# Optimization experiments

Measured on AMD Instinct MI355X. Metric: run time of the kernel, lower is better.

The kernel has to match this reference:

```python
import jax, jax.numpy as jnp
import numpy as np

D, NH, HD, NL, NP, DFF = 256, 8, 32, 4, 4, 1024
B, LQ = 16, 900
SHAPES = np.array([[100, 100], [50, 50], [25, 25], [13, 13]], dtype=np.int64)
_AREAS = SHAPES[:, 0] * SHAPES[:, 1]
LSI = np.concatenate([[0], np.cumsum(_AREAS)[:-1]]).astype(np.int64)
S = int(_AREAS.sum())  # 13294


def setup_inputs() -> dict:
    key = jax.random.key(0)
    ki = iter(jax.random.split(key, 40))
    def nrm(shape, s=1.0):
        return jax.random.normal(next(ki), shape, jnp.float32) * s
    p = dict(
        tgt=nrm((B, LQ, D)),
        query_pos=nrm((B, LQ, D)) * 0.1,
        reference_points=jax.random.uniform(next(ki), (B, LQ, NL, 2), jnp.float32),
        src=nrm((B, S, D)),
        src_spatial_shapes=SHAPES,
        level_start_index=LSI,
        src_padding_mask=np.zeros((B, S), dtype=bool),
        Wq=nrm((D, D), 0.02), bq=jnp.zeros((D,)),
        Wk=nrm((D, D), 0.02), bk=jnp.zeros((D,)),
        Wv=nrm((D, D), 0.02), bv=jnp.zeros((D,)),
        Wo=nrm((D, D), 0.02), bo=jnp.zeros((D,)),
        g2=jnp.ones((D,)), be2=jnp.zeros((D,)),
        Woff=nrm((D, NH * NL * NP * 2), 0.02),
        boff=jax.random.uniform(next(ki), (NH * NL * NP * 2,), jnp.float32, -0.5, 0.5),
        Waw=nrm((D, NH * NL * NP), 0.02), baw=jnp.zeros((NH * NL * NP,)),
        Wval=nrm((D, D), 0.02), bval=jnp.zeros((D,)),
        Wout=nrm((D, D), 0.02), bout=jnp.zeros((D,)),
        g1=jnp.ones((D,)), be1=jnp.zeros((D,)),
        W1f=nrm((D, DFF), 0.02), b1f=jnp.zeros((DFF,)),
        W2f=nrm((DFF, D), 0.02), b2f=jnp.zeros((D,)),
        g3=jnp.ones((D,)), be3=jnp.zeros((D,)),
    )
    return p


def layernorm(x, g, b):
    m = jnp.mean(x, -1, keepdims=True)
    v = jnp.var(x, -1, keepdims=True)
    return (x - m) * jax.lax.rsqrt(v + 1e-5) * g + b


def reference(tgt, query_pos, reference_points, src, src_spatial_shapes,
              level_start_index, src_padding_mask,
              Wq, bq, Wk, bk, Wv, bv, Wo, bo, g2, be2,
              Woff, boff, Waw, baw, Wval, bval, Wout, bout, g1, be1,
              W1f, b1f, W2f, b2f, g3, be3):
    Bq, Lq, _ = tgt.shape
    # ---- self-attention (q = k = tgt + pos, v = tgt), dropout in eval = identity
    q = tgt + query_pos
    qh = (q @ Wq + bq).reshape(Bq, Lq, NH, HD)
    kh = (q @ Wk + bk).reshape(Bq, Lq, NH, HD)
    vh = (tgt @ Wv + bv).reshape(Bq, Lq, NH, HD)
    att = jax.nn.softmax(jnp.einsum('bqhd,bkhd->bhqk', qh, kh) / np.sqrt(HD), axis=-1)
    sa = jnp.einsum('bhqk,bkhd->bqhd', att, vh).reshape(Bq, Lq, D) @ Wo + bo
    tgt = layernorm(tgt + sa, g2, be2)
    # ---- multi-scale deformable cross-attention
    query = tgt + query_pos
    value = src @ Wval + bval
    value = jnp.where(jnp.asarray(src_padding_mask)[..., None], 0.0, value)
    value = value.reshape(Bq, -1, NH, HD)
    off = (query @ Woff + boff).reshape(Bq, Lq, NH, NL, NP, 2)
    aw = jax.nn.softmax((query @ Waw + baw).reshape(Bq, Lq, NH, NL * NP), axis=-1)
    aw = aw.reshape(Bq, Lq, NH, NL, NP)
    ss = np.asarray(src_spatial_shapes)
    lsi = np.asarray(level_start_index)
    norm = jnp.asarray(ss[:, ::-1].astype(np.float32))  # (W, H) per level
    # sampling locations in [0,1]: [B, Lq, NH, NL, NP, 2]
    loc = reference_points[:, :, None, :, None, :] + off / norm[None, None, None, :, None, :]
    out = jnp.zeros((Bq, NH, Lq, HD), value.dtype)
    for l in range(NL):
        Hc, Wc = int(ss[l, 0]), int(ss[l, 1])
        v2 = value[:, lsi[l]:lsi[l] + Hc * Wc].transpose(0, 2, 1, 3)  # [B, NH, H*W, HD]
        x = loc[:, :, :, l, :, 0] * Wc - 0.5  # [B, Lq, NH, NP] (align_corners=False)
        y = loc[:, :, :, l, :, 1] * Hc - 0.5
        x0 = jnp.floor(x); y0 = jnp.floor(y)
        lx = x - x0; ly = y - y0
        x0i = x0.astype(jnp.int32); y0i = y0.astype(jnp.int32)
        samp = jnp.zeros((Bq, NH, Lq * NP, HD), value.dtype)
        for dy, dx, w in ((0, 0, (1 - ly) * (1 - lx)), (0, 1, (1 - ly) * lx),
                          (1, 0, ly * (1 - lx)), (1, 1, ly * lx)):
            xi = x0i + dx; yi = y0i + dy
            valid = (xi >= 0) & (xi < Wc) & (yi >= 0) & (yi < Hc)  # zero padding
            idx = jnp.clip(yi, 0, Hc - 1) * Wc + jnp.clip(xi, 0, Wc - 1)
            idx2 = idx.transpose(0, 2, 1, 3).reshape(Bq, NH, Lq * NP)
            g = jnp.take_along_axis(v2, idx2[..., None], axis=2)  # [B, NH, Lq*NP, HD]
            wv = (w * valid).transpose(0, 2, 1, 3).reshape(Bq, NH, Lq * NP)
            samp = samp + wv[..., None] * g
        samp = samp.reshape(Bq, NH, Lq, NP, HD)
        out = out + jnp.einsum('bqhp,bhqpd->bhqd', aw[:, :, :, l, :], samp)
    ca = out.transpose(0, 2, 1, 3).reshape(Bq, Lq, D) @ Wout + bout
    tgt = layernorm(tgt + ca, g1, be1)
    # ---- FFN
    ff = jax.nn.relu(tgt @ W1f + b1f) @ W2f + b2f
    return layernorm(tgt + ff, g3, be3)
```

## Files before the change

kernel.cpp:

```cpp
#include <hip/hip_runtime.h>
#include <math.h>

#define DD 256
#define NH 8
#define HD 32
#define NL 4
#define NP 4
#define DFF 1024
#define BB 16
#define LQ 900
#define S_TOT 13294

#define M1   (BB * LQ)
#define MP1  14464
#define MV   (BB * S_TOT)
#define MPV  212736

typedef unsigned short u16;
typedef unsigned int   u32;
typedef __attribute__((ext_vector_type(8))) short s8v;
typedef __attribute__((ext_vector_type(4))) float f32x4;

__constant__ int c_H[NL]    = {100, 50, 25, 13};
__constant__ int c_W[NL]    = {100, 50, 25, 13};
__constant__ int c_base[NL] = {0, 10000, 12500, 13125};

__device__ __forceinline__ float b2f(u16 u) {
    return __uint_as_float(((u32)u) << 16);
}
__device__ __forceinline__ u16 f2b(float f) {
    u32 x = __float_as_uint(f);
    u32 r = x + 0x7fffu + ((x >> 16) & 1u);
    return (u16)(r >> 16);
}
__device__ __forceinline__ u32 pk2(float a, float b) {
    return (u32)f2b(a) | ((u32)f2b(b) << 16);
}
__device__ __forceinline__ void gload16(const u16* g, u16* ldsbase) {
    __builtin_amdgcn_global_load_lds(
        (const __attribute__((address_space(1))) unsigned int*)(const void*)g,
        (__attribute__((address_space(3))) unsigned int*)(void*)ldsbase,
        16, 0, 0);
}
__device__ __forceinline__ int2 xcd_swizzle()
{
    int nwg  = gridDim.x * gridDim.y;
    int orig = blockIdx.y * gridDim.x + blockIdx.x;
    int q = nwg >> 3, r = nwg & 7;
    int xcd = orig & 7, pos = orig >> 3;
    int wg = (xcd < r ? xcd * (q + 1) : r * (q + 1) + (xcd - r) * q) + pos;
    int2 res;
    res.x = wg % gridDim.x;
    res.y = wg / gridDim.x;
    return res;
}

#define OFF_QK   0
#define OFF_V    131072
#define OFF_O    196608
#define OFF_VAL  262144
#define OFF_OUT  327680
#define OFF_OA   393216
#define OFF_F1   491520
#define OFF_F2   753664
#define WTS_TOT  1015808

__global__ __launch_bounds__(256)
void prep_kernel(const float* __restrict__ Wq, const float* __restrict__ Wk,
                 const float* __restrict__ Wv, const float* __restrict__ Wo,
                 const float* __restrict__ Wval, const float* __restrict__ Wout,
                 const float* __restrict__ Woff, const float* __restrict__ Waw,
                 const float* __restrict__ W1f, const float* __restrict__ W2f,
                 const float* __restrict__ pbq, const float* __restrict__ pbk,
                 const float* __restrict__ boff, const float* __restrict__ baw,
                 u16* __restrict__ WTS, float* __restrict__ bqk, float* __restrict__ boa)
{
    int t = blockIdx.x;
    if (t >= 992) {
        if (t == 992) {
            for (int i = threadIdx.x; i < 512; i += 256)
                bqk[i] = (i < 256) ? pbq[i] : pbk[i - 256];
        } else {
            for (int i = threadIdx.x; i < 384; i += 256)
                boa[i] = (i < 256) ? boff[i] : baw[i - 256];
        }
        return;
    }
    const float* src; u16* dst; int K, N, tt;
    if (t < 448) {
        int wsel = t >> 6; tt = t & 63;
        const float* srcs[7] = {Wq, Wk, Wv, Wo, Wval, Wout, Woff};
        const int   offs[7]  = {OFF_QK, OFF_QK + 65536, OFF_V, OFF_O, OFF_VAL, OFF_OUT, OFF_OA};
        src = srcs[wsel]; dst = WTS + offs[wsel]; K = 256; N = 256;
    } else if (t < 480) {
        tt = t - 448; src = Waw; dst = WTS + OFF_OA + 65536; K = 256; N = 128;
    } else if (t < 736) {
        tt = t - 480; src = W1f; dst = WTS + OFF_F1; K = 256; N = 1024;
    } else {
        tt = t - 736; src = W2f; dst = WTS + OFF_F2; K = 1024; N = 256;
    }
    int nt = N / 32;
    int n0 = (tt % nt) * 32, k0 = (tt / nt) * 32;

    __shared__ float tb[32][33];
    int tx = threadIdx.x & 31, ty = threadIdx.x >> 5;
    #pragma unroll
    for (int i = 0; i < 4; ++i) {
        int k = ty + i * 8;
        tb[k][tx] = src[(size_t)(k0 + k) * N + n0 + tx];
    }
    __syncthreads();
    #pragma unroll
    for (int i = 0; i < 4; ++i) {
        int n = ty + i * 8;
        dst[(size_t)(n0 + n) * K + k0 + tx] = f2b(tb[tx][n]);
    }
}

__global__ __launch_bounds__(256)
void acvt2_kernel(const float* __restrict__ tgt, const float* __restrict__ qpos,
                  u16* __restrict__ B0, u16* __restrict__ B1)
{
    int i8 = blockIdx.x * 256 + threadIdx.x;
    int row = i8 >> 5;
    uint4 o0, o1;
    if (row < M1) {
        const float4* tp = (const float4*)(tgt + (size_t)i8 * 8);
        const float4* pp = (const float4*)(qpos + (size_t)i8 * 8);
        float4 t0 = tp[0], t1 = tp[1], p0 = pp[0], p1 = pp[1];
        o1.x = pk2(t0.x, t0.y); o1.y = pk2(t0.z, t0.w);
        o1.z = pk2(t1.x, t1.y); o1.w = pk2(t1.z, t1.w);
        o0.x = pk2(t0.x + p0.x, t0.y + p0.y); o0.y = pk2(t0.z + p0.z, t0.w + p0.w);
        o0.z = pk2(t1.x + p1.x, t1.y + p1.y); o0.w = pk2(t1.z + p1.z, t1.w + p1.w);
    } else {
        o0.x = o0.y = o0.z = o0.w = 0;
        o1 = o0;
    }
    ((uint4*)B0)[i8] = o0;
    ((uint4*)B1)[i8] = o1;
}

template<int BNT, int OUTBF, int RELU>
__global__ __launch_bounds__(256)
void mgemm(const u16* __restrict__ A, const u16* __restrict__ Bt,
           const float* __restrict__ bias, void* __restrict__ Cv,
           int K, int N, int Mreal)
{
    constexpr int MF = (BNT == 128) ? 4 : 2;
    __shared__ u16 Asu[2][128 * 32];
    __shared__ u16 Bsu[2][BNT * 32];

    int2 sw = xcd_swizzle();
    int tid = threadIdx.x;
    int w = tid >> 6, l = tid & 63;
    int mbase = (BNT == 128) ? (w >> 1) * 64 : w * 32;
    int nbase = (BNT == 128) ? (w & 1) * 64 : 0;
    long m0 = (long)sw.y * 128;
    int n0 = sw.x * BNT;

    f32x4 acc[MF][4];
    #pragma unroll
    for (int i = 0; i < MF; ++i)
        #pragma unroll
        for (int j = 0; j < 4; ++j) {
            acc[i][j][0] = 0.f; acc[i][j][1] = 0.f;
            acc[i][j][2] = 0.f; acc[i][j][3] = 0.f;
        }

    int lr = l & 15, lk = (l >> 4) * 8;
    int srow = l >> 2;
    int scol = (l & 3) * 8;

    auto stage = [&](int buf, int k0) {
        if (BNT == 128) {
            #pragma unroll
            for (int j = 0; j < 2; ++j) {
                int row = w * 32 + j * 16;
                gload16(Bt + (size_t)(n0 + row + srow) * K + k0 + scol, &Bsu[buf][row * 32]);
            }
        } else {
            int row = w * 16;
            gload16(Bt + (size_t)(n0 + row + srow) * K + k0 + scol, &Bsu[buf][row * 32]);
        }
        #pragma unroll
        for (int j = 0; j < 2; ++j) {
            int row = w * 32 + j * 16;
            gload16(A + (m0 + row + srow) * (long)K + k0 + scol, &Asu[buf][row * 32]);
        }
    };

    int nsteps = K >> 5;
    stage(0, 0);
    __syncthreads();

    int cur = 0;
    for (int s = 0; s < nsteps; ++s) {
        if (s + 1 < nsteps) stage(cur ^ 1, (s + 1) * 32);
        s8v af[MF], bf[4];
        #pragma unroll
        for (int mi = 0; mi < MF; ++mi)
            af[mi] = *(const s8v*)(Asu[cur] + (mbase + mi * 16 + lr) * 32 + lk);
        #pragma unroll
        for (int nj = 0; nj < 4; ++nj)
            bf[nj] = *(const s8v*)(Bsu[cur] + (nbase + nj * 16 + lr) * 32 + lk);
        #pragma unroll
        for (int mi = 0; mi < MF; ++mi)
            #pragma unroll
            for (int nj = 0; nj < 4; ++nj)
                acc[mi][nj] = __builtin_amdgcn_mfma_f32_16x16x32_bf16(
                    af[mi], bf[nj], acc[mi][nj], 0, 0, 0);
        __syncthreads();
        cur ^= 1;
    }

    int lq = l >> 4;
    #pragma unroll
    for (int nj = 0; nj < 4; ++nj) {
        int col = n0 + nbase + nj * 16 + lr;
        float bv = bias[col];
        #pragma unroll
        for (int mi = 0; mi < MF; ++mi) {
            #pragma unroll
            for (int r = 0; r < 4; ++r) {
                long row = m0 + mbase + mi * 16 + lq * 4 + r;
                float v = acc[mi][nj][r] + bv;
                if (RELU) v = fmaxf(v, 0.f);
                if (OUTBF) ((u16*)Cv)[row * N + col] = f2b(v);
                else       ((float*)Cv)[row * N + col] = v;
            }
        }
    }
}

__global__ __launch_bounds__(256)
void vgemm(const float* __restrict__ A, const u16* __restrict__ Bt,
           const float* __restrict__ bias, u16* __restrict__ C, int Mreal)
{
    const int K = 256, N = 256;
    __shared__ u16 Asu[64 * 32];
    __shared__ u16 Bsu[128 * 32];

    int2 sw = xcd_swizzle();
    int tid = threadIdx.x;
    int w = tid >> 6, l = tid & 63;
    int wr = w >> 1, wc = w & 1;
    long m0 = (long)sw.y * 64;
    int n0 = sw.x * 128;

    f32x4 acc[2][4];
    #pragma unroll
    for (int i = 0; i < 2; ++i)
        #pragma unroll
        for (int j = 0; j < 4; ++j) {
            acc[i][j][0] = 0.f; acc[i][j][1] = 0.f;
            acc[i][j][2] = 0.f; acc[i][j][3] = 0.f;
        }

    int lr = l & 15, lk = (l >> 4) * 8;
    int srow = l >> 2, scol = (l & 3) * 8;

    for (int k0 = 0; k0 < K; k0 += 32) {
        #pragma unroll
        for (int j = 0; j < 2; ++j) {
            int row = w * 32 + j * 16;
            gload16(Bt + (size_t)(n0 + row + srow) * K + k0 + scol, &Bsu[row * 32]);
        }
        int c = tid;
        #pragma unroll
        for (int it = 0; it < 2; ++it) {
            int row = c >> 3, col = (c & 7) * 4;
            long gr = m0 + row;
            if (gr >= Mreal) gr = Mreal - 1;
            float4 v = *(const float4*)(A + gr * K + k0 + col);
            ushort4 o;
            o.x = f2b(v.x); o.y = f2b(v.y); o.z = f2b(v.z); o.w = f2b(v.w);
            ((ushort4*)Asu)[c] = o;
            c += 256;
        }
        __syncthreads();
        s8v af[2], bf[4];
        #pragma unroll
        for (int mi = 0; mi < 2; ++mi)
            af[mi] = *(const s8v*)(Asu + (wr * 32 + mi * 16 + lr) * 32 + lk);
        #pragma unroll
        for (int nj = 0; nj < 4; ++nj)
            bf[nj] = *(const s8v*)(Bsu + (wc * 64 + nj * 16 + lr) * 32 + lk);
        #pragma unroll
        for (int mi = 0; mi < 2; ++mi)
            #pragma unroll
            for (int nj = 0; nj < 4; ++nj)
                acc[mi][nj] = __builtin_amdgcn_mfma_f32_16x16x32_bf16(
                    af[mi], bf[nj], acc[mi][nj], 0, 0, 0);
        __syncthreads();
    }

    int lq = l >> 4;
    #pragma unroll
    for (int nj = 0; nj < 4; ++nj) {
        int col = n0 + wc * 64 + nj * 16 + lr;
        float bv = bias[col];
        #pragma unroll
        for (int mi = 0; mi < 2; ++mi) {
            #pragma unroll
            for (int r = 0; r < 4; ++r) {
                long row = m0 + wr * 32 + mi * 16 + lq * 4 + r;
                C[row * N + col] = f2b(acc[mi][nj][r] + bv);
            }
        }
    }
}

#define QT 64
#define KT2 64
#define KSP 48
#define VSP 40
#define PSP 72
__global__ __launch_bounds__(256)
void mattn(const u16* __restrict__ qk, const u16* __restrict__ vh,
           u16* __restrict__ sa)
{
    __shared__ u16 Ks[KT2][KSP];
    __shared__ u32 Vt32[32][VSP];
    __shared__ u16 Ps[4][16][PSP];

    int tid = threadIdx.x;
    int w = tid >> 6, l = tid & 63;
    int lr = l & 15, hi = l >> 4;
    int b = blockIdx.x >> 3, h = blockIdx.x & 7;
    int q0 = blockIdx.y * QT + w * 16;

    s8v qf;
    {
        s8v raw = *(const s8v*)(qk + ((size_t)(b * LQ + q0 + lr) * 512) + h * HD + hi * 8);
        #pragma unroll
        for (int j = 0; j < 8; ++j)
            raw[j] = (short)f2b(b2f((u16)raw[j]) * 0.17677669529663687f);
        qf = raw;
    }

    f32x4 o0 = {0.f,0.f,0.f,0.f}, o1 = {0.f,0.f,0.f,0.f};
    float lrun[4] = {0.f,0.f,0.f,0.f};

    const u16* kbase = qk + (size_t)b * LQ * 512 + 256 + h * HD;
    const u16* vbase = vh + (size_t)b * LQ * 256 + h * HD;

    int krow = tid >> 2, kc8 = (tid & 3) * 8;
    int k2 = tid & 31, d0 = (tid >> 5) * 4;

    for (int kb = 0; kb < LQ; kb += KT2) {
        int gk = kb + krow;        if (gk >= LQ) gk = LQ - 1;
        int gv0 = kb + 2 * k2;     if (gv0 >= LQ) gv0 = LQ - 1;
        int gv1 = kb + 2 * k2 + 1; if (gv1 >= LQ) gv1 = LQ - 1;
        uint4 kv = *(const uint4*)(kbase + (size_t)gk * 512 + kc8);
        uint2 va = *(const uint2*)(vbase + (size_t)gv0 * 256 + d0);
        uint2 vb = *(const uint2*)(vbase + (size_t)gv1 * 256 + d0);
        __syncthreads();
        *(uint4*)(&Ks[krow][kc8]) = kv;
        Vt32[d0 + 0][k2] = (va.x & 0xffffu)      | (vb.x << 16);
        Vt32[d0 + 1][k2] = (va.x >> 16)          | (vb.x & 0xffff0000u);
        Vt32[d0 + 2][k2] = (va.y & 0xffffu)      | (vb.y << 16);
        Vt32[d0 + 3][k2] = (va.y >> 16)          | (vb.y & 0xffff0000u);
        __syncthreads();

        f32x4 s[4];
        #pragma unroll
        for (int kk = 0; kk < 4; ++kk) {
            s8v bk = *(const s8v*)(&Ks[kk * 16 + lr][hi * 8]);
            f32x4 z = {0.f,0.f,0.f,0.f};
            s[kk] = __builtin_amdgcn_mfma_f32_16x16x32_bf16(qf, bk, z, 0, 0, 0);
        }
        if (kb + KT2 > LQ) {
            #pragma unroll
            for (int kk = 0; kk < 4; ++kk)
                if (kb + kk * 16 + lr >= LQ) {
                    s[kk][0] = -1e30f; s[kk][1] = -1e30f;
                    s[kk][2] = -1e30f; s[kk][3] = -1e30f;
                }
        }

        #pragma unroll
        for (int r = 0; r < 4; ++r) {
            float p0 = __expf(s[0][r]);
            float p1 = __expf(s[1][r]);
            float p2 = __expf(s[2][r]);
            float p3 = __expf(s[3][r]);
            lrun[r] += (p0 + p1) + (p2 + p3);
            int qr = hi * 4 + r;
            Ps[w][qr][lr]      = f2b(p0);
            Ps[w][qr][16 + lr] = f2b(p1);
            Ps[w][qr][32 + lr] = f2b(p2);
            Ps[w][qr][48 + lr] = f2b(p3);
        }

        s8v ap0  = *(const s8v*)(&Ps[w][lr][hi * 8]);
        s8v ap1  = *(const s8v*)(&Ps[w][lr][32 + hi * 8]);
        s8v bv00 = *(const s8v*)(&Vt32[lr][hi * 4]);
        s8v bv10 = *(const s8v*)(&Vt32[lr][16 + hi * 4]);
        s8v bv01 = *(const s8v*)(&Vt32[16 + lr][hi * 4]);
        s8v bv11 = *(const s8v*)(&Vt32[16 + lr][16 + hi * 4]);
        o0 = __builtin_amdgcn_mfma_f32_16x16x32_bf16(ap0, bv00, o0, 0, 0, 0);
        o0 = __builtin_amdgcn_mfma_f32_16x16x32_bf16(ap1, bv10, o0, 0, 0, 0);
        o1 = __builtin_amdgcn_mfma_f32_16x16x32_bf16(ap0, bv01, o1, 0, 0, 0);
        o1 = __builtin_amdgcn_mfma_f32_16x16x32_bf16(ap1, bv11, o1, 0, 0, 0);
    }

    #pragma unroll
    for (int r = 0; r < 4; ++r) {
        float ps = lrun[r];
        ps += __shfl_xor(ps, 1);
        ps += __shfl_xor(ps, 2);
        ps += __shfl_xor(ps, 4);
        ps += __shfl_xor(ps, 8);
        int q = q0 + hi * 4 + r;
        if (q < LQ) {
            float inv = 1.f / ps;
            u16* op = sa + (size_t)(b * LQ + q) * DD + h * HD;
            op[lr]      = f2b(o0[r] * inv);
            op[16 + lr] = f2b(o1[r] * inv);
        }
    }
}

__global__ __launch_bounds__(256)
void ln_kernel(const float* __restrict__ x, const u16* __restrict__ y,
               const float* __restrict__ g, const float* __restrict__ be,
               float* __restrict__ out, const float* __restrict__ pos,
               u16* __restrict__ bfout, int M)
{
    int wave = threadIdx.x >> 6;
    int lane = threadIdx.x & 63;
    int row = blockIdx.x * 4 + wave;
    if (row >= M) return;
    float4 xv = ((const float4*)(x + (size_t)row * DD))[lane];
    ushort4 yv = ((const ushort4*)(y + (size_t)row * DD))[lane];
    float v[4] = {xv.x + b2f(yv.x), xv.y + b2f(yv.y),
                  xv.z + b2f(yv.z), xv.w + b2f(yv.w)};
    float s = v[0] + v[1] + v[2] + v[3];
    float sq = v[0]*v[0] + v[1]*v[1] + v[2]*v[2] + v[3]*v[3];
    for (int o = 32; o; o >>= 1) {
        s += __shfl_xor(s, o);
        sq += __shfl_xor(sq, o);
    }
    float mean = s * (1.f / DD);
    float var = sq * (1.f / DD) - mean * mean;
    float r = rsqrtf(var + 1e-5f);
    float4 gv = ((const float4*)g)[lane];
    float4 bv = ((const float4*)be)[lane];
    float4 ov;
    ov.x = (v[0] - mean) * r * gv.x + bv.x;
    ov.y = (v[1] - mean) * r * gv.y + bv.y;
    ov.z = (v[2] - mean) * r * gv.z + bv.z;
    ov.w = (v[3] - mean) * r * gv.w + bv.w;
    ((float4*)(out + (size_t)row * DD))[lane] = ov;
    if (bfout) {
        float4 pv = make_float4(0.f, 0.f, 0.f, 0.f);
        if (pos) pv = ((const float4*)(pos + (size_t)row * DD))[lane];
        ushort4 bo;
        bo.x = f2b(ov.x + pv.x); bo.y = f2b(ov.y + pv.y);
        bo.z = f2b(ov.z + pv.z); bo.w = f2b(ov.w + pv.w);
        ((ushort4*)(bfout + (size_t)row * DD))[lane] = bo;
    }
}

__global__ __launch_bounds__(256)
void sample_kernel(const float* __restrict__ offaw, const float* __restrict__ refp,
                   const u16* __restrict__ value, u16* __restrict__ out)
{
    __shared__ float2 sPW[2][128][4];
    int t = threadIdx.x;
    int sub = t >> 7;
    int bq = blockIdx.x * 2 + sub;
    int b = bq / LQ;

    {
        int pt = t & 127;
        int h = pt >> 4, j = pt & 15, l = j >> 2, p = j & 3;
        const float* row = offaw + (size_t)bq * 384;
        float lg = row[256 + h * 16 + j];
        float mx = lg;
        mx = fmaxf(mx, __shfl_xor(mx, 1));
        mx = fmaxf(mx, __shfl_xor(mx, 2));
        mx = fmaxf(mx, __shfl_xor(mx, 4));
        mx = fmaxf(mx, __shfl_xor(mx, 8));
        float e = __expf(lg - mx);
        float se = e;
        se += __shfl_xor(se, 1);
        se += __shfl_xor(se, 2);
        se += __shfl_xor(se, 4);
        se += __shfl_xor(se, 8);
        float aw = e / se;

        float ox = row[h * 32 + l * 8 + p * 2 + 0];
        float oy = row[h * 32 + l * 8 + p * 2 + 1];
        int Hc = c_H[l], Wc = c_W[l];
        float x = refp[(size_t)bq * 8 + l * 2 + 0] * Wc + ox - 0.5f;
        float y = refp[(size_t)bq * 8 + l * 2 + 1] * Hc + oy - 0.5f;
        float x0f = floorf(x), y0f = floorf(y);
        float lx = x - x0f, ly = y - y0f;
        int x0 = (int)x0f, y0 = (int)y0f;
        int vb = (b * S_TOT + c_base[l]) * 128;
        #pragma unroll
        for (int c = 0; c < 4; ++c) {
            int dy = c >> 1, dx = c & 1;
            int xi = x0 + dx, yi = y0 + dy;
            bool ok = (xi >= 0) & (xi < Wc) & (yi >= 0) & (yi < Hc);
            float wgt = (dy ? ly : 1.f - ly) * (dx ? lx : 1.f - lx) * aw;
            float2 pw;
            pw.x = __int_as_float(ok ? vb + (yi * Wc + xi) * 128 : 0);
            pw.y = ok ? wgt : 0.f;
            sPW[sub][pt][c] = pw;
        }
    }
    __syncthreads();

    {
        int s = t & 127;
        int h = s >> 4, d2 = s & 15;
        const u32* v32 = (const u32*)value;
        int lane = h * 16 + d2;
        float a0 = 0.f, a1 = 0.f;
        #pragma unroll
        for (int j = 0; j < 16; ++j) {
            #pragma unroll
            for (int c = 0; c < 4; ++c) {
                float2 pw = sPW[sub][h * 16 + j][c];
                u32 pv = v32[__float_as_int(pw.x) + lane];
                a0 += pw.y * __uint_as_float(pv << 16);
                a1 += pw.y * __uint_as_float(pv & 0xffff0000u);
            }
        }
        *(u32*)(out + (size_t)bq * DD + h * 32 + d2 * 2) = pk2(a0, a1);
    }
}

extern "C" void kernel_launch(void* const* d_in, const int* in_sizes, int n_in,
                              void* d_out, int out_size, void* d_ws, size_t ws_size,
                              hipStream_t stream)
{
    const float* tgt  = (const float*)d_in[0];
    const float* qpos = (const float*)d_in[1];
    const float* refp = (const float*)d_in[2];
    const float* src  = (const float*)d_in[3];
    const float* Wq  = (const float*)d_in[7];
    const float* pbq = (const float*)d_in[8];
    const float* Wk  = (const float*)d_in[9];
    const float* pbk = (const float*)d_in[10];
    const float* Wv  = (const float*)d_in[11];
    const float* pbv = (const float*)d_in[12];
    const float* Wo  = (const float*)d_in[13];
    const float* pbo = (const float*)d_in[14];
    const float* g2  = (const float*)d_in[15];
    const float* be2 = (const float*)d_in[16];
    const float* Woff = (const float*)d_in[17];
    const float* boff = (const float*)d_in[18];
    const float* Waw  = (const float*)d_in[19];
    const float* baw  = (const float*)d_in[20];
    const float* Wval = (const float*)d_in[21];
    const float* bval = (const float*)d_in[22];
    const float* Wout = (const float*)d_in[23];
    const float* bout = (const float*)d_in[24];
    const float* g1   = (const float*)d_in[25];
    const float* be1  = (const float*)d_in[26];
    const float* W1f  = (const float*)d_in[27];
    const float* b1f  = (const float*)d_in[28];
    const float* W2f  = (const float*)d_in[29];
    const float* b2f_ = (const float*)d_in[30];
    const float* g3   = (const float*)d_in[31];
    const float* be3  = (const float*)d_in[32];

    char* base = (char*)d_ws;
    size_t off = 0;
    auto alloc = [&](size_t bytes) -> void* {
        void* p = base + off;
        off = (off + bytes + 255) & ~(size_t)255;
        return p;
    };
    const size_t AB = (size_t)MP1 * DD * sizeof(u16);
    u16* B0  = (u16*)alloc(AB);
    u16* B1  = (u16*)alloc(AB);
    u16* BQK = (u16*)alloc((size_t)MP1 * 512 * sizeof(u16));
    u16* B4  = (u16*)alloc(AB);
    u16* TMPB= (u16*)alloc(AB);
    u16* FFH = (u16*)alloc((size_t)MP1 * DFF * sizeof(u16));
    u16* VAL = (u16*)alloc((size_t)MPV * DD * sizeof(u16));
    float* F0 = (float*)alloc((size_t)MP1 * 384 * sizeof(float));
    float* F2 = (float*)alloc((size_t)MP1 * DD * sizeof(float));
    float* F3 = (float*)alloc((size_t)MP1 * DD * sizeof(float));
    u16* WTS = (u16*)alloc((size_t)WTS_TOT * sizeof(u16));
    float* bqk = (float*)alloc(512 * sizeof(float));
    float* boa = (float*)alloc(384 * sizeof(float));

    dim3 blk(256);

    prep_kernel<<<dim3(994), blk, 0, stream>>>(
        Wq, Wk, Wv, Wo, Wval, Wout, Woff, Waw, W1f, W2f,
        pbq, pbk, boff, baw, WTS, bqk, boa);

    const int MT = MP1 / 128;
    const dim3 gval(2, MPV / 64);
    const dim3 g512b(8,  MT);
    const dim3 g256b(4,  MT);
    const dim3 g384b(6,  MT);
    const dim3 g1kb(16,  MT);

    acvt2_kernel<<<dim3(MP1 * 32 / 256), blk, 0, stream>>>(tgt, qpos, B0, B1);
    mgemm<64,1,0><<<g512b, blk, 0, stream>>>(B0, WTS + OFF_QK, bqk, BQK, DD, 512, M1);
    mgemm<64,1,0><<<g256b, blk, 0, stream>>>(B1, WTS + OFF_V, pbv, B4, DD, DD, M1);
    mattn<<<dim3(BB * NH, (LQ + QT - 1) / QT), blk, 0, stream>>>(BQK, B4, B0);
    mgemm<64,1,0><<<g256b, blk, 0, stream>>>(B0, WTS + OFF_O, pbo, TMPB, DD, DD, M1);
    ln_kernel<<<dim3(M1 / 4), blk, 0, stream>>>(tgt, TMPB, g2, be2, F2, qpos, B1, M1);

    vgemm<<<gval, blk, 0, stream>>>(src, WTS + OFF_VAL, bval, VAL, MV);
    mgemm<64,0,0><<<g384b, blk, 0, stream>>>(B1, WTS + OFF_OA, boa, F0, DD, 384, M1);
    sample_kernel<<<dim3(M1 / 2), blk, 0, stream>>>(F0, refp, VAL, B4);
    mgemm<64,1,0><<<g256b, blk, 0, stream>>>(B4, WTS + OFF_OUT, bout, TMPB, DD, DD, M1);
    ln_kernel<<<dim3(M1 / 4), blk, 0, stream>>>(F2, TMPB, g1, be1, F3, nullptr, B1, M1);

    mgemm<64,1,1><<<g1kb, blk, 0, stream>>>(B1, WTS + OFF_F1, b1f, FFH, DD, DFF, M1);
    mgemm<64,1,0><<<g256b, blk, 0, stream>>>(FFH, WTS + OFF_F2, b2f_, TMPB, DFF, DD, M1);
    ln_kernel<<<dim3(M1 / 4), blk, 0, stream>>>(F3, TMPB, g3, be3, (float*)d_out, nullptr, nullptr, M1);
}
```

Before: 313.8 us.

## Widen deformable sampling gathers to 8 bytes and split points across half-warps

The sampling kernel now gathers four bf16 channels per 8-byte load instead of two per 4-byte load. Each thread handles half of a head's 16 sampling points, and the two halves are combined through a shared-memory reduction with an extra block barrier. This is meant to cut the number of scattered gather instructions while keeping thread-level parallelism. The self-attention kernel also raises wave priority around its MFMA blocks with s_setprio, so matrix work is issued ahead of other waves' memory traffic.

After: 320.0 us. Within noise of the previous version (+2.0%).

```diff
diff --git a/kernel.cpp b/kernel.cpp
--- a/kernel.cpp
+++ b/kernel.cpp
@@ -363,12 +363,14 @@
         __syncthreads();
 
         f32x4 s[4];
+        __builtin_amdgcn_s_setprio(1);
         #pragma unroll
         for (int kk = 0; kk < 4; ++kk) {
             s8v bk = *(const s8v*)(&Ks[kk * 16 + lr][hi * 8]);
             f32x4 z = {0.f,0.f,0.f,0.f};
             s[kk] = __builtin_amdgcn_mfma_f32_16x16x32_bf16(qf, bk, z, 0, 0, 0);
         }
+        __builtin_amdgcn_s_setprio(0);
         if (kb + KT2 > LQ) {
             #pragma unroll
             for (int kk = 0; kk < 4; ++kk)
@@ -398,10 +400,12 @@
         s8v bv10 = *(const s8v*)(&Vt32[lr][16 + hi * 4]);
         s8v bv01 = *(const s8v*)(&Vt32[16 + lr][hi * 4]);
         s8v bv11 = *(const s8v*)(&Vt32[16 + lr][16 + hi * 4]);
+        __builtin_amdgcn_s_setprio(1);
         o0 = __builtin_amdgcn_mfma_f32_16x16x32_bf16(ap0, bv00, o0, 0, 0, 0);
         o0 = __builtin_amdgcn_mfma_f32_16x16x32_bf16(ap1, bv10, o0, 0, 0, 0);
         o1 = __builtin_amdgcn_mfma_f32_16x16x32_bf16(ap0, bv01, o1, 0, 0, 0);
         o1 = __builtin_amdgcn_mfma_f32_16x16x32_bf16(ap1, bv11, o1, 0, 0, 0);
+        __builtin_amdgcn_s_setprio(0);
     }
 
     #pragma unroll
@@ -467,6 +471,7 @@
                    const u16* __restrict__ value, u16* __restrict__ out)
 {
     __shared__ float2 sPW[2][128][4];
+    __shared__ float4 sRed[2][64];
     int t = threadIdx.x;
     int sub = t >> 7;
     int bq = blockIdx.x * 2 + sub;
@@ -498,7 +503,7 @@
         float x0f = floorf(x), y0f = floorf(y);
         float lx = x - x0f, ly = y - y0f;
         int x0 = (int)x0f, y0 = (int)y0f;
-        int vb = (b * S_TOT + c_base[l]) * 128;
+        int vb = (b * S_TOT + c_base[l]) * 64;
         #pragma unroll
         for (int c = 0; c < 4; ++c) {
             int dy = c >> 1, dx = c & 1;
@@ -506,30 +511,44 @@
             bool ok = (xi >= 0) & (xi < Wc) & (yi >= 0) & (yi < Hc);
             float wgt = (dy ? ly : 1.f - ly) * (dx ? lx : 1.f - lx) * aw;
             float2 pw;
-            pw.x = __int_as_float(ok ? vb + (yi * Wc + xi) * 128 : 0);
+            pw.x = __int_as_float(ok ? vb + (yi * Wc + xi) * 64 : 0);
             pw.y = ok ? wgt : 0.f;
             sPW[sub][pt][c] = pw;
         }
     }
     __syncthreads();
 
+    int ts = t & 127;
+    int jh = ts >> 6;
+    int s6 = ts & 63;
+    int h = s6 >> 3, d4 = s6 & 7;
     {
-        int s = t & 127;
-        int h = s >> 4, d2 = s & 15;
-        const u32* v32 = (const u32*)value;
-        int lane = h * 16 + d2;
-        float a0 = 0.f, a1 = 0.f;
-        #pragma unroll
-        for (int j = 0; j < 16; ++j) {
+        const uint2* v64 = (const uint2*)value;
+        int lane = h * 8 + d4;
+        float a0 = 0.f, a1 = 0.f, a2 = 0.f, a3 = 0.f;
+        #pragma unroll
+        for (int jj = 0; jj < 8; ++jj) {
+            int pt = h * 16 + jh * 8 + jj;
             #pragma unroll
             for (int c = 0; c < 4; ++c) {
-                float2 pw = sPW[sub][h * 16 + j][c];
-                u32 pv = v32[__float_as_int(pw.x) + lane];
-                a0 += pw.y * __uint_as_float(pv << 16);
-                a1 += pw.y * __uint_as_float(pv & 0xffff0000u);
+                float2 pw = sPW[sub][pt][c];
+                uint2 g = v64[__float_as_int(pw.x) + lane];
+                a0 += pw.y * __uint_as_float(g.x << 16);
+                a1 += pw.y * __uint_as_float(g.x & 0xffff0000u);
+                a2 += pw.y * __uint_as_float(g.y << 16);
+                a3 += pw.y * __uint_as_float(g.y & 0xffff0000u);
             }
         }
-        *(u32*)(out + (size_t)bq * DD + h * 32 + d2 * 2) = pk2(a0, a1);
+        if (jh == 1) sRed[sub][s6] = make_float4(a0, a1, a2, a3);
+        __syncthreads();
+        if (jh == 0) {
+            float4 p = sRed[sub][s6];
+            a0 += p.x; a1 += p.y; a2 += p.z; a3 += p.w;
+            uint2 o;
+            o.x = pk2(a0, a1);
+            o.y = pk2(a2, a3);
+            *(uint2*)(out + (size_t)bq * DD + h * 32 + d4 * 4) = o;
+        }
     }
 }
 
```
